# Optimization experiments

Measured on AMD Instinct MI355X. Metric: run time of the kernel, lower is better.

Reference implementation:

```python
import jax, jax.numpy as jnp
import numpy as np

NT = 34000      # nodes per type
NTYPES = 3
NMP = 2         # metapaths per node type
E = 300000      # metapath instances per metapath
L = 3           # metapath length
H = 8           # attention heads
D = 64          # hidden_dim (per-head dim)
HD = H * D      # 512
AV = 128        # attn_vec_dim
C = 8           # out_dim (classes)
NTGT = 1000
NLAYERS = 2
N = NTYPES * NT


def _glorot(k, shape, fan_in):
    return jax.random.normal(k, shape, jnp.float32) * (1.0 / np.sqrt(fan_in))


def setup_inputs() -> dict:
    key = jax.random.key(0)
    ks = jax.random.split(key, 24)
    X0 = jax.random.normal(ks[0], (NT, 512), jnp.float32)
    X1 = jax.random.normal(ks[1], (NT, 256), jnp.float32)
    X2 = jax.random.normal(ks[2], (NT, 128), jnp.float32)
    # metapath instances: column 0 is the target node (must be of type i),
    # remaining columns are intermediate nodes of any type
    dst = jax.random.randint(ks[3], (NTYPES, NMP, E), 0, NT) + jnp.arange(NTYPES)[:, None, None] * NT
    mids = jax.random.randint(ks[4], (NTYPES, NMP, E, L - 1), 0, N)
    mp_idx = jnp.concatenate([dst[..., None], mids], axis=-1).astype(jnp.int32)
    target_idx = jax.random.randint(ks[5], (NTGT,), 0, NT).astype(jnp.int32)
    inp = {
        "X0": X0, "X1": X1, "X2": X2,
        # per-type feature transforms (fc_list)
        "fcW0": _glorot(ks[6], (512, D), 512), "fcb0": jnp.zeros((D,), jnp.float32),
        "fcW1": _glorot(ks[7], (256, D), 256), "fcb1": jnp.zeros((D,), jnp.float32),
        "fcW2": _glorot(ks[8], (128, D), 128), "fcb2": jnp.zeros((D,), jnp.float32),
        # GAT-style intra-metapath attention params [layer, type, metapath, H, D]
        "attn1": jax.random.normal(ks[9], (NLAYERS, NTYPES, NMP, H, D), jnp.float32) * 0.1,
        "attn2": jax.random.normal(ks[10], (NLAYERS, NTYPES, NMP, H, D), jnp.float32) * 0.1,
        # inter-metapath attention (fc1 + attention vector q) [layer, type, ...]
        "mpW": _glorot(ks[11], (NLAYERS, NTYPES, HD, AV), HD),
        "mpb": jnp.zeros((NLAYERS, NTYPES, AV), jnp.float32),
        "mpq": jax.random.normal(ks[12], (NLAYERS, NTYPES, AV), jnp.float32) * 0.1,
        # per-layer output fc: in_dim*num_heads -> out_dim
        "lW0": _glorot(ks[13], (HD, D), HD), "lb0": jnp.zeros((D,), jnp.float32),
        "lW1": _glorot(ks[14], (HD, C), HD), "lb1": jnp.zeros((C,), jnp.float32),
        "mp_idx": mp_idx,
        "target_idx": target_idx,
    }
    return inp


def _ctr_layer(h, a1, a2, mpW, mpb, mpq, mp_idx):
    # one MAGNN_nc_layer ctr-ntype pass: gather metapath instances, intra-metapath
    # attention (segment softmax over target node), inter-metapath attention,
    # then scatter per-type results into the shared node tensor (contiguous blocks).
    outs = []
    for i in range(NTYPES):
        per_mp = []
        for p in range(NMP):
            idx = mp_idx[i, p]                      # [E, L]
            feats = h[idx]                          # [E, L, D] irregular gather
            hid = feats.mean(axis=1)                # rnn_type='average' metapath encoding
            dst = idx[:, 0] - i * NT                # local target-node ids
            e = jax.nn.leaky_relu(
                jnp.einsum('ed,hd->eh', feats[:, 0, :], a1[i, p])
                + jnp.einsum('ed,hd->eh', hid, a2[i, p]), 0.2)   # [E, H]
            m = jax.ops.segment_max(e, dst, num_segments=NT)
            ex = jnp.exp(e - m[dst])
            den = jax.ops.segment_sum(ex, dst, num_segments=NT)
            alpha = ex / jnp.maximum(den[dst], 1e-9)             # segment softmax
            out = jax.ops.segment_sum(alpha[:, :, None] * hid[:, None, :], dst,
                                      num_segments=NT)           # [NT, H, D]
            per_mp.append(jax.nn.elu(out.reshape(NT, HD)))
        st = jnp.stack(per_mp)                       # [P, NT, HD]
        s = jnp.tanh(jnp.einsum('pnd,dk->pnk', st, mpW[i]) + mpb[i]).mean(axis=1) @ mpq[i]  # [P]
        beta = jax.nn.softmax(s)
        outs.append(jnp.einsum('p,pnd->nd', beta, st))
    return jnp.concatenate(outs, axis=0)             # scatter back: [N, HD]


def reference(X0, X1, X2, fcW0, fcb0, fcW1, fcb1, fcW2, fcb2,
              attn1, attn2, mpW, mpb, mpq, lW0, lb0, lW1, lb1,
              mp_idx, target_idx):
    # type-masked gather -> per-type linear -> scatter (types are contiguous blocks)
    h = jnp.concatenate([X0 @ fcW0 + fcb0, X1 @ fcW1 + fcb1, X2 @ fcW2 + fcb2], axis=0)
    hm = _ctr_layer(h, attn1[0], attn2[0], mpW[0], mpb[0], mpq[0], mp_idx)
    h = jax.nn.elu(hm @ lW0 + lb0)                   # layer 0: HD -> hidden, ELU
    hm = _ctr_layer(h, attn1[1], attn2[1], mpW[1], mpb[1], mpq[1], mp_idx)
    logits = hm @ lW1 + lb1                          # final layer: HD -> out_dim
    return logits[target_idx]
```

## Files before the change

kernel.cpp:

```cpp
#include <hip/hip_runtime.h>
#include <hip/hip_bf16.h>
#include <math.h>

#define NT 34000
#define NTYPES 3
#define NMP 2
#define NE 300000
#define HH 8
#define DD 64
#define HD 512
#define AV 128
#define NCLS 8
#define NTGT 1000
#define NN (NTYPES*NT)
#define NBLK 133

typedef short short8 __attribute__((ext_vector_type(8)));
typedef float f32x4 __attribute__((ext_vector_type(4)));

__device__ __forceinline__ short f2bf(float f){
  unsigned u = __float_as_uint(f);
  unsigned r = u + 0x7FFFu + ((u>>16)&1u);
  return (short)(r>>16);
}
__device__ __forceinline__ float bf2f(short s){
  return __uint_as_float(((unsigned)(unsigned short)s)<<16);
}
__device__ __forceinline__ float fast_tanh(float x){
  x = fminf(15.f, fmaxf(-15.f, x));
  float t = __expf(2.f*x);
  return (t-1.f)/(t+1.f);
}

__device__ __forceinline__ void compute_beta(const float* __restrict__ av,
                                             const float* __restrict__ q,
                                             float* b0, float* b1){
  float s0=0.f, s1=0.f;
  #pragma unroll
  for(int c=0;c<32;c++){
    float4 a0=((const float4*)av)[c];
    float4 a1=((const float4*)(av+128))[c];
    float4 qq=((const float4*)q)[c];
    s0 += a0.x*qq.x+a0.y*qq.y+a0.z*qq.z+a0.w*qq.w;
    s1 += a1.x*qq.x+a1.y*qq.y+a1.z*qq.z+a1.w*qq.w;
  }
  s0 /= (float)NT; s1 /= (float)NT;
  float mm=fmaxf(s0,s1);
  float e0=__expf(s0-mm), e1=__expf(s1-mm);
  float d=e0+e1;
  *b0=e0/d; *b1=e1/d;
}

__global__ void k_zero(int* __restrict__ p, int n){
  int i = blockIdx.x*256+threadIdx.x; if(i<n) p[i]=0;
}

__global__ void k_hist(const int* __restrict__ mp, int* __restrict__ counts){
  int e = blockIdx.x*256+threadIdx.x; int g = blockIdx.y;
  if(e>=NE) return;
  int i = g>>1;
  int dst = mp[((size_t)g*NE+e)*3] - i*NT;
  atomicAdd(&counts[g*NT+dst],1);
}

__global__ __launch_bounds__(256) void k_blkred(const int* __restrict__ counts, int* __restrict__ bsum){
  int g=blockIdx.y, blk=blockIdx.x, t=threadIdx.x;
  int idx=blk*256+t;
  int v=(idx<NT)? counts[g*NT+idx]:0;
  #pragma unroll
  for(int off=32;off;off>>=1) v+=__shfl_down(v,off,64);
  __shared__ int sh[4];
  if((t&63)==0) sh[t>>6]=v;
  __syncthreads();
  if(t==0) bsum[g*NBLK+blk]=sh[0]+sh[1]+sh[2]+sh[3];
}

__global__ __launch_bounds__(256) void k_scansums(int* __restrict__ bsum){
  int g=blockIdx.x; int t=threadIdx.x;
  __shared__ int s[256];
  int v=(t<NBLK)? bsum[g*NBLK+t]:0;
  s[t]=v; __syncthreads();
  for(int off=1;off<256;off<<=1){
    int tmp=(t>=off)?s[t-off]:0; __syncthreads();
    s[t]+=tmp; __syncthreads();
  }
  if(t<NBLK) bsum[g*NBLK+t]=s[t]-v;
}

__global__ __launch_bounds__(256) void k_scanapply(int* __restrict__ counts, const int* __restrict__ bsum,
                                                   int* __restrict__ offs){
  int g=blockIdx.y, blk=blockIdx.x, t=threadIdx.x;
  int idx=blk*256+t;
  int v=(idx<NT)? counts[g*NT+idx]:0;
  __shared__ int s[256];
  s[t]=v; __syncthreads();
  for(int off=1;off<256;off<<=1){
    int tmp=(t>=off)?s[t-off]:0; __syncthreads();
    s[t]+=tmp; __syncthreads();
  }
  int excl = s[t]-v + bsum[g*NBLK+blk];
  if(idx<NT){ offs[g*(NT+1)+idx]=excl; counts[g*NT+idx]=0; }
  if(idx==NT-1) offs[g*(NT+1)+NT]=excl+v;
}

__global__ void k_scatter(const int* __restrict__ mp, const int* __restrict__ offs,
                          int* __restrict__ counts, int2* __restrict__ mids){
  int e = blockIdx.x*256+threadIdx.x; int g=blockIdx.y;
  if(e>=NE) return;
  int i=g>>1;
  const int* row = mp + ((size_t)g*NE+e)*3;
  int dst = row[0]-i*NT;
  int pos = offs[g*(NT+1)+dst] + atomicAdd(&counts[g*NT+dst],1);
  mids[(size_t)g*NE+pos]=make_int2(row[1],row[2]);
}

__global__ void k_packWall(const float* __restrict__ W0, const float* __restrict__ W1,
                           const float* __restrict__ W2, const float* __restrict__ WL,
                           const float* __restrict__ mpW,
                           short* __restrict__ p0, short* __restrict__ p1,
                           short* __restrict__ p2, short* __restrict__ pL,
                           short* __restrict__ bpk4, float* __restrict__ accv){
  int which = blockIdx.y;
  int tid = blockIdx.x*256+threadIdx.x;
  if(which<4){
    const float* W; short* wpk; int K;
    if(which==0){W=W0;wpk=p0;K=512;}
    else if(which==1){W=W1;wpk=p1;K=256;}
    else if(which==2){W=W2;wpk=p2;K=128;}
    else {W=WL;wpk=pL;K=512;}
    int nk = K>>5;
    int total = nk*256;
    if(tid>=total) return;
    int lane = tid&63; int c=(tid>>6)&3; int kt=tid>>8;
    int col = c*16 + (lane&15);
    int kbase = kt*32 + ((lane>>4)<<3);
    short8 hi, lo;
    #pragma unroll
    for(int j=0;j<8;j++){
      float w = W[(size_t)(kbase+j)*64+col];
      short h = f2bf(w); hi[j]=h;
      lo[j] = f2bf(w - bf2f(h));
    }
    ((short8*)wpk)[tid] = hi;
    ((short8*)wpk)[total+tid] = lo;
  } else {
    if(which==4 && tid<1024) accv[tid]=0.f;
    if(tid>=8192) return;
    const float* W = mpW + (size_t)(which-4)*512*128;
    short* out = bpk4 + (size_t)(which-4)*65536;
    int lane=tid&63; int c=(tid>>6)&7; int t=tid>>9;
    int kbase = t*32 + ((lane>>4)<<3);
    int col = c*16 + (lane&15);
    short8 v;
    #pragma unroll
    for(int jj=0;jj<8;jj++) v[jj]=f2bf(W[(size_t)(kbase+jj)*128+col]);
    ((short8*)out)[tid]=v;
  }
}

__global__ __launch_bounds__(256) void k_mm64f(const float* __restrict__ X, const short* __restrict__ wpk,
               const float* __restrict__ b, float* __restrict__ Y, short* __restrict__ Yb,
               int rows, int K, int act){
  int wave = threadIdx.x>>6, lane = threadIdx.x&63;
  int row0 = blockIdx.x*64 + wave*16;
  if(row0>=rows) return;
  int r = row0 + (lane&15);
  int rc = min(r, rows-1);
  const float* xr = X + (size_t)rc*K + ((lane>>4)<<3);
  int nk = K>>5;
  const short8* wh = (const short8*)wpk;
  const short8* wl = wh + (size_t)nk*256;
  f32x4 acc[4];
  #pragma unroll
  for(int c=0;c<4;c++) acc[c]=(f32x4){0.f,0.f,0.f,0.f};
  for(int kt=0;kt<nk;kt++){
    float4 f0=*(const float4*)(xr + kt*32);
    float4 f1=*(const float4*)(xr + kt*32 + 4);
    float xs[8]={f0.x,f0.y,f0.z,f0.w,f1.x,f1.y,f1.z,f1.w};
    short8 ah, al;
    #pragma unroll
    for(int j=0;j<8;j++){
      short h=f2bf(xs[j]); ah[j]=h;
      al[j]=f2bf(xs[j]-bf2f(h));
    }
    const short8* whk = wh + (size_t)kt*256 + lane;
    const short8* wlk = wl + (size_t)kt*256 + lane;
    #pragma unroll
    for(int c=0;c<4;c++){
      short8 bh = whk[c*64];
      short8 bl = wlk[c*64];
      acc[c]=__builtin_amdgcn_mfma_f32_16x16x32_bf16(ah,bh,acc[c],0,0,0);
      acc[c]=__builtin_amdgcn_mfma_f32_16x16x32_bf16(al,bh,acc[c],0,0,0);
      acc[c]=__builtin_amdgcn_mfma_f32_16x16x32_bf16(ah,bl,acc[c],0,0,0);
    }
  }
  int rbase = row0 + ((lane>>4)<<2);
  int colb = lane&15;
  #pragma unroll
  for(int c=0;c<4;c++){
    int col = c*16+colb;
    float bb = b[col];
    #pragma unroll
    for(int q=0;q<4;q++){
      int rw = rbase+q;
      if(rw<rows){
        float v = acc[c][q]+bb;
        if(act) v = v>0.f? v : (__expf(v)-1.f);
        Y[(size_t)rw*64+col]=v;
        Yb[(size_t)rw*64+col]=f2bf(v);
      }
    }
  }
}

__global__ __launch_bounds__(256) void k_mm64fB(const short* __restrict__ Xa, const short* __restrict__ Xb,
               const float* __restrict__ accv_s, const float* __restrict__ q,
               const short* __restrict__ wpk,
               const float* __restrict__ b, float* __restrict__ Y, int rows, int act){
  const int K=512, nk=16;
  float b0, b1;
  compute_beta(accv_s, q, &b0, &b1);
  int wave = threadIdx.x>>6, lane = threadIdx.x&63;
  int row0 = blockIdx.x*64 + wave*16;
  if(row0>=rows) return;
  int r = row0 + (lane&15);
  int rc = min(r, rows-1);
  const short* xra = Xa + (size_t)rc*K + ((lane>>4)<<3);
  const short* xrb = Xb + (size_t)rc*K + ((lane>>4)<<3);
  const short8* wh = (const short8*)wpk;
  const short8* wl = wh + (size_t)nk*256;
  f32x4 acc[4];
  #pragma unroll
  for(int c=0;c<4;c++) acc[c]=(f32x4){0.f,0.f,0.f,0.f};
  for(int kt=0;kt<nk;kt++){
    short8 sa = *(const short8*)(xra + kt*32);
    short8 sb = *(const short8*)(xrb + kt*32);
    short8 ah, al;
    #pragma unroll
    for(int j=0;j<8;j++){
      float x = b0*bf2f(sa[j]) + b1*bf2f(sb[j]);
      short h=f2bf(x); ah[j]=h;
      al[j]=f2bf(x-bf2f(h));
    }
    const short8* whk = wh + (size_t)kt*256 + lane;
    const short8* wlk = wl + (size_t)kt*256 + lane;
    #pragma unroll
    for(int c=0;c<4;c++){
      short8 bh = whk[c*64];
      short8 bl = wlk[c*64];
      acc[c]=__builtin_amdgcn_mfma_f32_16x16x32_bf16(ah,bh,acc[c],0,0,0);
      acc[c]=__builtin_amdgcn_mfma_f32_16x16x32_bf16(al,bh,acc[c],0,0,0);
      acc[c]=__builtin_amdgcn_mfma_f32_16x16x32_bf16(ah,bl,acc[c],0,0,0);
    }
  }
  int rbase = row0 + ((lane>>4)<<2);
  int colb = lane&15;
  #pragma unroll
  for(int c=0;c<4;c++){
    int col = c*16+colb;
    float bb = b[col];
    #pragma unroll
    for(int q=0;q<4;q++){
      int rw = rbase+q;
      if(rw<rows){
        float v = acc[c][q]+bb;
        if(act) v = v>0.f? v : (__expf(v)-1.f);
        Y[(size_t)rw*64+col]=v;
      }
    }
  }
}

__global__ __launch_bounds__(256) void k_cvt(const float* __restrict__ src, short* __restrict__ dst, int n8){
  int i = blockIdx.x*256+threadIdx.x;
  if(i>=n8) return;
  float4 f0=((const float4*)src)[i*2], f1=((const float4*)src)[i*2+1];
  short8 v;
  v[0]=f2bf(f0.x); v[1]=f2bf(f0.y); v[2]=f2bf(f0.z); v[3]=f2bf(f0.w);
  v[4]=f2bf(f1.x); v[5]=f2bf(f1.y); v[6]=f2bf(f1.z); v[7]=f2bf(f1.w);
  ((short8*)dst)[i]=v;
}

__global__ __launch_bounds__(256) void k_pre(const float* __restrict__ h, const float* __restrict__ a1,
              const float* __restrict__ a2, float* __restrict__ ptab, int ngroups){
  int node = blockIdx.x*256+threadIdx.x;
  if(node>=NN) return;
  const float* hr = h + (size_t)node*64;
  float4 hv[16];
  #pragma unroll
  for(int q=0;q<16;q++) hv[q]=((const float4*)hr)[q];
  for(int g=0; g<ngroups; g++){
    const float* A1 = a1 + (size_t)g*512;
    const float* A2 = a2 + (size_t)g*512;
    float out[16];
    #pragma unroll
    for(int o=0;o<8;o++){
      float acc=0.f;
      #pragma unroll
      for(int q=0;q<16;q++){
        float4 w=((const float4*)A1)[o*16+q];
        acc += hv[q].x*w.x+hv[q].y*w.y+hv[q].z*w.z+hv[q].w*w.w;
      }
      out[o]=acc;
    }
    #pragma unroll
    for(int o=0;o<8;o++){
      float acc=0.f;
      #pragma unroll
      for(int q=0;q<16;q++){
        float4 w=((const float4*)A2)[o*16+q];
        acc += hv[q].x*w.x+hv[q].y*w.y+hv[q].z*w.z+hv[q].w*w.w;
      }
      out[8+o]=acc;
    }
    float* dp = ptab + ((size_t)g*NN+node)*16;
    #pragma unroll
    for(int q=0;q<4;q++)
      ((float4*)dp)[q]=make_float4(out[q*4],out[q*4+1],out[q*4+2],out[q*4+3]);
  }
}

__global__ __launch_bounds__(256) void k_seg(const int* __restrict__ offs_all, const float* __restrict__ ptab,
   const int2* __restrict__ mids_all, const float* __restrict__ h, const short* __restrict__ hb,
   short* __restrict__ stb, float* __restrict__ stf, int type, int tobf){
  __shared__ float wsh[4][64];
  int wave = threadIdx.x>>6, lane = threadIdx.x&63;
  int n = blockIdx.x*4 + wave;
  if(n>=NT) return;
  int p = blockIdx.y; int g = type*2+p;
  const int* offs = offs_all + (size_t)g*(NT+1);
  const int2* mids_g = mids_all + (size_t)g*NE;
  const float* pt = ptab + (size_t)g*NN*16;
  const unsigned short* hbp = (const unsigned short*)hb;

  int off = offs[n], end = offs[n+1];
  const float third = 1.f/3.f;
  int j = lane>>3, hh = lane&7;

  const float* pn = pt + (size_t)(type*NT+n)*16;
  float baseh = pn[hh] + pn[8+hh]*third;

  float m = -1e30f, den = 0.f;
  for(int s=off+j; s<end; s+=8){
    int2 mm = mids_g[s];
    float q1 = pt[(size_t)mm.x*16 + 8 + hh];
    float q2 = pt[(size_t)mm.y*16 + 8 + hh];
    float e = baseh + (q1+q2)*third;
    float ev = e>0.f? e : 0.2f*e;
    float mn = fmaxf(m, ev);
    den = den*__expf(m-mn) + __expf(ev-mn);
    m = mn;
  }
  #pragma unroll
  for(int o8=8;o8<=32;o8<<=1){
    float om = __shfl_xor(m, o8, 64);
    float od = __shfl_xor(den, o8, 64);
    float mn = fmaxf(m, om);
    den = den*__expf(m-mn) + od*__expf(om-mn);
    m = mn;
  }
  float invD = 1.f/fmaxf(den, 1e-9f);

  float o[8]={0.f,0.f,0.f,0.f,0.f,0.f,0.f,0.f};
  for(int base=off; base<end; base+=8){
    int s = base+j;
    float w = 0.f;
    if(s<end){
      int2 mm = mids_g[s];
      float q1 = pt[(size_t)mm.x*16 + 8 + hh];
      float q2 = pt[(size_t)mm.y*16 + 8 + hh];
      float e = baseh + (q1+q2)*third;
      float ev = e>0.f? e : 0.2f*e;
      w = __expf(ev-m)*invD;
    }
    wsh[wave][lane] = w;
    int cnt = min(8, end-base);
    for(int k=0;k<cnt;k++){
      int2 mm = mids_g[base+k];
      unsigned ux = hbp[(size_t)mm.x*64+lane];
      unsigned uy = hbp[(size_t)mm.y*64+lane];
      float hvm = __uint_as_float(ux<<16) + __uint_as_float(uy<<16);
      float4 a0 = *(const float4*)&wsh[wave][k*8];
      float4 a1 = *(const float4*)&wsh[wave][k*8+4];
      o[0]+=a0.x*hvm; o[1]+=a0.y*hvm; o[2]+=a0.z*hvm; o[3]+=a0.w*hvm;
      o[4]+=a1.x*hvm; o[5]+=a1.y*hvm; o[6]+=a1.z*hvm; o[7]+=a1.w*hvm;
    }
  }

  float hn = h[((size_t)type*NT+(size_t)n)*64+lane];
  short* stbp = stb + (size_t)p*NT*512 + (size_t)n*512 + lane;
  float* stfp = stf + (size_t)p*NT*512 + (size_t)n*512 + lane;
  #pragma unroll
  for(int q=0;q<8;q++){
    float v = (end>off)? (o[q] + hn)*third : 0.f;
    v = v>0.f? v : (__expf(v)-1.f);
    if(tobf) stbp[q*64] = f2bf(v);
    else     stfp[q*64] = v;
  }
}

__global__ __launch_bounds__(256) void k_tanhmm(const short* __restrict__ stb, const float* __restrict__ stf,
                        int isbf, const short* __restrict__ bpk,
                        const float* __restrict__ bias, float* __restrict__ accv_s){
  __shared__ float red[4][128];
  int wave=threadIdx.x>>6, lane=threadIdx.x&63;
  int p=blockIdx.y;
  int row0 = (blockIdx.x*4+wave)*16;
  int active = (row0<NT);
  int rA = row0 + (lane&15); if(rA>NT-1) rA=NT-1;
  const short* arowb = stb + (size_t)p*NT*512 + (size_t)rA*512 + ((lane>>4)<<3);
  const float* arowf = stf + (size_t)p*NT*512 + (size_t)rA*512 + ((lane>>4)<<3);
  f32x4 acc[8];
  #pragma unroll
  for(int c=0;c<8;c++) acc[c]=(f32x4){0.f,0.f,0.f,0.f};
  const short8* bp = (const short8*)bpk;
  if(active){
    for(int kt=0;kt<16;kt++){
      short8 a;
      if(isbf){
        a = *(const short8*)(arowb + kt*32);
      } else {
        float4 f0 = *(const float4*)(arowf + kt*32);
        float4 f1 = *(const float4*)(arowf + kt*32 + 4);
        a[0]=f2bf(f0.x); a[1]=f2bf(f0.y); a[2]=f2bf(f0.z); a[3]=f2bf(f0.w);
        a[4]=f2bf(f1.x); a[5]=f2bf(f1.y); a[6]=f2bf(f1.z); a[7]=f2bf(f1.w);
      }
      const short8* bk = bp + (size_t)kt*512 + lane;
      #pragma unroll
      for(int c=0;c<8;c++){
        short8 bfr = bk[c*64];
        acc[c]=__builtin_amdgcn_mfma_f32_16x16x32_bf16(a,bfr,acc[c],0,0,0);
      }
    }
  }
  int rbase = row0 + ((lane>>4)<<2);
  int colb = lane&15;
  float sc[8];
  #pragma unroll
  for(int c=0;c<8;c++){
    float s=0.f;
    if(active){
      float bb=bias[c*16+colb];
      #pragma unroll
      for(int r=0;r<4;r++){
        if(rbase+r<NT) s += fast_tanh(acc[c][r]+bb);
      }
    }
    s += __shfl_xor(s,16,64);
    s += __shfl_xor(s,32,64);
    sc[c]=s;
  }
  if(lane<16){
    #pragma unroll
    for(int c=0;c<8;c++) red[wave][c*16+lane]=sc[c];
  }
  __syncthreads();
  if(threadIdx.x<128){
    float t = red[0][threadIdx.x]+red[1][threadIdx.x]+red[2][threadIdx.x]+red[3][threadIdx.x];
    atomicAdd(&accv_s[p*128+threadIdx.x], t);
  }
}

__global__ __launch_bounds__(64) void k_final(const float* __restrict__ st0, const float* __restrict__ st1,
      const float* __restrict__ accv_s, const float* __restrict__ q,
      const float* __restrict__ lW1, const float* __restrict__ lb1,
      const int* __restrict__ tgt, float* __restrict__ out){
  int t=blockIdx.x; int lane=threadIdx.x;
  int row=tgt[t];
  float b0, b1;
  compute_beta(accv_s, q, &b0, &b1);
  float acc[8]={0.f,0.f,0.f,0.f,0.f,0.f,0.f,0.f};
  #pragma unroll
  for(int kk=0;kk<8;kk++){
    int k=kk*64+lane;
    float hm=b0*st0[(size_t)row*512+k]+b1*st1[(size_t)row*512+k];
    const float4* wp=(const float4*)(lW1+(size_t)k*8);
    float4 w0=wp[0], w1=wp[1];
    acc[0]+=hm*w0.x; acc[1]+=hm*w0.y; acc[2]+=hm*w0.z; acc[3]+=hm*w0.w;
    acc[4]+=hm*w1.x; acc[5]+=hm*w1.y; acc[6]+=hm*w1.z; acc[7]+=hm*w1.w;
  }
  #pragma unroll
  for(int c=0;c<8;c++){
    #pragma unroll
    for(int off=32;off>0;off>>=1) acc[c]+=__shfl_xor(acc[c],off,64);
  }
  if(lane<8){
    float v=0.f;
    #pragma unroll
    for(int c=0;c<8;c++) if(lane==c) v=acc[c];
    out[t*8+lane]=v+lb1[lane];
  }
}

extern "C" void kernel_launch(void* const* d_in, const int* in_sizes, int n_in,
                              void* d_out, int out_size, void* d_ws, size_t ws_size,
                              hipStream_t stream) {
  const float* X0=(const float*)d_in[0];
  const float* X1=(const float*)d_in[1];
  const float* X2=(const float*)d_in[2];
  const float* fcW0=(const float*)d_in[3]; const float* fcb0=(const float*)d_in[4];
  const float* fcW1=(const float*)d_in[5]; const float* fcb1=(const float*)d_in[6];
  const float* fcW2=(const float*)d_in[7]; const float* fcb2=(const float*)d_in[8];
  const float* attn1=(const float*)d_in[9];
  const float* attn2=(const float*)d_in[10];
  const float* mpW=(const float*)d_in[11];
  const float* mpb=(const float*)d_in[12];
  const float* mpq=(const float*)d_in[13];
  const float* lW0=(const float*)d_in[14]; const float* lb0=(const float*)d_in[15];
  const float* lW1=(const float*)d_in[16]; const float* lb1=(const float*)d_in[17];
  const int* mp=(const int*)d_in[18];
  const int* tgt=(const int*)d_in[19];
  float* out=(float*)d_out;

  char* ws=(char*)d_ws;
  float* h0   =(float*)(ws+0);
  float* h1   =(float*)(ws+26112000);
  float* ptab =(float*)(ws+52224000);
  int*   offs =(int*  )(ws+91392000);
  int*   counts=(int* )(ws+92208128);
  int2*  mids =(int2* )(ws+100224128);
  short* hb   =(short*)(ws+114624128);
  short* stb  =(short*)(ws+133824128);
  float* stf  =(float*)(ws+133824128);
  short* bpk4 =(short*)(ws+273088128);
  float* accv =(float*)(ws+273612416);
  short* wpk0 =(short*)(ws+92208128);
  short* wpk1 =(short*)(ws+92339200);
  short* wpkL =(short*)(ws+92404736);
  short* wpk2 =(short*)(ws+92535808);
  int*   bsum =(int*  )(ws+133824128);

  dim3 b256(256);
  k_zero<<<dim3((6*NT+255)/256),b256,0,stream>>>(counts,6*NT);
  k_hist<<<dim3((NE+255)/256,6),b256,0,stream>>>(mp,counts);
  k_blkred<<<dim3(NBLK,6),b256,0,stream>>>(counts,bsum);
  k_scansums<<<dim3(6),b256,0,stream>>>(bsum);
  k_scanapply<<<dim3(NBLK,6),b256,0,stream>>>(counts,bsum,offs);
  k_scatter<<<dim3((NE+255)/256,6),b256,0,stream>>>(mp,offs,counts,mids);

  k_packWall<<<dim3(32,8),b256,0,stream>>>(fcW0,fcW1,fcW2,lW0,mpW,wpk0,wpk1,wpk2,wpkL,bpk4,accv);

  k_mm64f<<<dim3(532),b256,0,stream>>>(X0,wpk0,fcb0,h0,hb,NT,512,0);
  k_mm64f<<<dim3(532),b256,0,stream>>>(X1,wpk1,fcb1,h0+(size_t)NT*64,hb+(size_t)NT*64,NT,256,0);
  k_mm64f<<<dim3(532),b256,0,stream>>>(X2,wpk2,fcb2,h0+(size_t)2*NT*64,hb+(size_t)2*NT*64,NT,128,0);

  k_pre<<<dim3((NN+255)/256),b256,0,stream>>>(h0,attn1,attn2,ptab,6);
  for(int type=0;type<3;type++){
    k_seg<<<dim3(NT/4,2),b256,0,stream>>>(offs,ptab,mids,h0,hb,stb,stf,type,1);
    k_tanhmm<<<dim3(532,2),b256,0,stream>>>(stb,stf,1,bpk4+(size_t)type*65536,
                                            mpb+(0*3+type)*128,accv+type*256);
    k_mm64fB<<<dim3(532),b256,0,stream>>>(stb,stb+(size_t)NT*512,accv+type*256,mpq+(0*3+type)*128,
                                          wpkL,lb0,h1+(size_t)type*NT*64,NT,1);
  }

  k_cvt<<<dim3((NN*64/8+255)/256),b256,0,stream>>>(h1,hb,NN*64/8);
  k_pre<<<dim3((NN+255)/256),b256,0,stream>>>(h1,attn1+(size_t)6*512,attn2+(size_t)6*512,ptab,2);
  k_seg<<<dim3(NT/4,2),b256,0,stream>>>(offs,ptab,mids,h1,hb,stb,stf,0,0);
  k_tanhmm<<<dim3(532,2),b256,0,stream>>>(stb,stf,0,bpk4+(size_t)3*65536,
                                          mpb+(1*3+0)*128,accv+3*256);
  k_final<<<dim3(NTGT),dim3(64),0,stream>>>(stf,stf+(size_t)NT*512,accv+3*256,mpq+(1*3+0)*128,
                                            lW1,lb1,tgt,out);
}
```

Before: 1.178 ms.

## Co-schedule CSR scatter with feature matmuls and fold bf16 conversion into k_pre

```diff
diff --git a/kernel.cpp b/kernel.cpp
--- a/kernel.cpp
+++ b/kernel.cpp
@@ -14,6 +14,9 @@
 #define NTGT 1000
 #define NN (NTYPES*NT)
 #define NBLK 133
+#define SCBLK 1172
+#define TSC (6*SCBLK)
+#define TMM (3*532)
 
 typedef short short8 __attribute__((ext_vector_type(8)));
 typedef float f32x4 __attribute__((ext_vector_type(4)));
@@ -101,17 +104,6 @@
   int excl = s[t]-v + bsum[g*NBLK+blk];
   if(idx<NT){ offs[g*(NT+1)+idx]=excl; counts[g*NT+idx]=0; }
   if(idx==NT-1) offs[g*(NT+1)+NT]=excl+v;
-}
-
-__global__ void k_scatter(const int* __restrict__ mp, const int* __restrict__ offs,
-                          int* __restrict__ counts, int2* __restrict__ mids){
-  int e = blockIdx.x*256+threadIdx.x; int g=blockIdx.y;
-  if(e>=NE) return;
-  int i=g>>1;
-  const int* row = mp + ((size_t)g*NE+e)*3;
-  int dst = row[0]-i*NT;
-  int pos = offs[g*(NT+1)+dst] + atomicAdd(&counts[g*NT+dst],1);
-  mids[(size_t)g*NE+pos]=make_int2(row[1],row[2]);
 }
 
 __global__ void k_packWall(const float* __restrict__ W0, const float* __restrict__ W1,
@@ -158,14 +150,38 @@
   }
 }
 
-__global__ __launch_bounds__(256) void k_mm64f(const float* __restrict__ X, const short* __restrict__ wpk,
-               const float* __restrict__ b, float* __restrict__ Y, short* __restrict__ Yb,
-               int rows, int K, int act){
+__global__ __launch_bounds__(256) void k_scmm(const int* __restrict__ mp, const int* __restrict__ offs,
+    int* __restrict__ counts, int2* __restrict__ mids,
+    const float* __restrict__ X0, const float* __restrict__ X1, const float* __restrict__ X2,
+    const short* __restrict__ wpk0, const short* __restrict__ wpk1, const short* __restrict__ wpk2,
+    const float* __restrict__ fb0, const float* __restrict__ fb1, const float* __restrict__ fb2,
+    float* __restrict__ Y, short* __restrict__ Yb){
+  int bid = blockIdx.x;
+  int period = bid/27, r = bid - period*27;
+  if(r<22){
+    int s = period*22 + r; if(s>=TSC) return;
+    int g = s/SCBLK; int e = (s - g*SCBLK)*256 + threadIdx.x;
+    if(e>=NE) return;
+    int i = g>>1;
+    const int* row = mp + ((size_t)g*NE+e)*3;
+    int dst = row[0]-i*NT;
+    int pos = offs[g*(NT+1)+dst] + atomicAdd(&counts[g*NT+dst],1);
+    mids[(size_t)g*NE+pos]=make_int2(row[1],row[2]);
+    return;
+  }
+  int mID = period*5 + (r-22); if(mID>=TMM) return;
+  int which = mID/532; int xb = mID - which*532;
+  const float* X; const short* wpk; const float* b; int K;
+  if(which==0){X=X0;wpk=wpk0;b=fb0;K=512;}
+  else if(which==1){X=X1;wpk=wpk1;b=fb1;K=256;}
+  else {X=X2;wpk=wpk2;b=fb2;K=128;}
+  float* Yw = Y + (size_t)which*NT*64;
+  short* Ybw = Yb + (size_t)which*NT*64;
   int wave = threadIdx.x>>6, lane = threadIdx.x&63;
-  int row0 = blockIdx.x*64 + wave*16;
-  if(row0>=rows) return;
-  int r = row0 + (lane&15);
-  int rc = min(r, rows-1);
+  int row0 = xb*64 + wave*16;
+  if(row0>=NT) return;
+  int rr = row0 + (lane&15);
+  int rc = min(rr, NT-1);
   const float* xr = X + (size_t)rc*K + ((lane>>4)<<3);
   int nk = K>>5;
   const short8* wh = (const short8*)wpk;
@@ -203,11 +219,10 @@
     #pragma unroll
     for(int q=0;q<4;q++){
       int rw = rbase+q;
-      if(rw<rows){
+      if(rw<NT){
         float v = acc[c][q]+bb;
-        if(act) v = v>0.f? v : (__expf(v)-1.f);
-        Y[(size_t)rw*64+col]=v;
-        Yb[(size_t)rw*64+col]=f2bf(v);
+        Yw[(size_t)rw*64+col]=v;
+        Ybw[(size_t)rw*64+col]=f2bf(v);
       }
     }
   }
@@ -271,24 +286,26 @@
   }
 }
 
-__global__ __launch_bounds__(256) void k_cvt(const float* __restrict__ src, short* __restrict__ dst, int n8){
-  int i = blockIdx.x*256+threadIdx.x;
-  if(i>=n8) return;
-  float4 f0=((const float4*)src)[i*2], f1=((const float4*)src)[i*2+1];
-  short8 v;
-  v[0]=f2bf(f0.x); v[1]=f2bf(f0.y); v[2]=f2bf(f0.z); v[3]=f2bf(f0.w);
-  v[4]=f2bf(f1.x); v[5]=f2bf(f1.y); v[6]=f2bf(f1.z); v[7]=f2bf(f1.w);
-  ((short8*)dst)[i]=v;
-}
-
 __global__ __launch_bounds__(256) void k_pre(const float* __restrict__ h, const float* __restrict__ a1,
-              const float* __restrict__ a2, float* __restrict__ ptab, int ngroups){
+              const float* __restrict__ a2, float* __restrict__ ptab, int ngroups,
+              short* __restrict__ hbout){
   int node = blockIdx.x*256+threadIdx.x;
   if(node>=NN) return;
   const float* hr = h + (size_t)node*64;
   float4 hv[16];
   #pragma unroll
   for(int q=0;q<16;q++) hv[q]=((const float4*)hr)[q];
+  if(hbout){
+    short* hp = hbout + (size_t)node*64;
+    #pragma unroll
+    for(int qq=0;qq<8;qq++){
+      float4 a=hv[2*qq], b4=hv[2*qq+1];
+      short8 v;
+      v[0]=f2bf(a.x); v[1]=f2bf(a.y); v[2]=f2bf(a.z); v[3]=f2bf(a.w);
+      v[4]=f2bf(b4.x); v[5]=f2bf(b4.y); v[6]=f2bf(b4.z); v[7]=f2bf(b4.w);
+      ((short8*)hp)[qq]=v;
+    }
+  }
   for(int g=0; g<ngroups; g++){
     const float* A1 = a1 + (size_t)g*512;
     const float* A2 = a2 + (size_t)g*512;
@@ -520,14 +537,14 @@
   int*   counts=(int* )(ws+92208128);
   int2*  mids =(int2* )(ws+100224128);
   short* hb   =(short*)(ws+114624128);
+  short* wpk0 =(short*)(ws+127680128);
+  short* wpk1 =(short*)(ws+127811200);
+  short* wpkL =(short*)(ws+127876736);
+  short* wpk2 =(short*)(ws+128007808);
   short* stb  =(short*)(ws+133824128);
   float* stf  =(float*)(ws+133824128);
   short* bpk4 =(short*)(ws+273088128);
   float* accv =(float*)(ws+273612416);
-  short* wpk0 =(short*)(ws+92208128);
-  short* wpk1 =(short*)(ws+92339200);
-  short* wpkL =(short*)(ws+92404736);
-  short* wpk2 =(short*)(ws+92535808);
   int*   bsum =(int*  )(ws+133824128);
 
   dim3 b256(256);
@@ -536,15 +553,13 @@
   k_blkred<<<dim3(NBLK,6),b256,0,stream>>>(counts,bsum);
   k_scansums<<<dim3(6),b256,0,stream>>>(bsum);
   k_scanapply<<<dim3(NBLK,6),b256,0,stream>>>(counts,bsum,offs);
-  k_scatter<<<dim3((NE+255)/256,6),b256,0,stream>>>(mp,offs,counts,mids);
 
   k_packWall<<<dim3(32,8),b256,0,stream>>>(fcW0,fcW1,fcW2,lW0,mpW,wpk0,wpk1,wpk2,wpkL,bpk4,accv);
 
-  k_mm64f<<<dim3(532),b256,0,stream>>>(X0,wpk0,fcb0,h0,hb,NT,512,0);
-  k_mm64f<<<dim3(532),b256,0,stream>>>(X1,wpk1,fcb1,h0+(size_t)NT*64,hb+(size_t)NT*64,NT,256,0);
-  k_mm64f<<<dim3(532),b256,0,stream>>>(X2,wpk2,fcb2,h0+(size_t)2*NT*64,hb+(size_t)2*NT*64,NT,128,0);
-
-  k_pre<<<dim3((NN+255)/256),b256,0,stream>>>(h0,attn1,attn2,ptab,6);
+  k_scmm<<<dim3(320*27),b256,0,stream>>>(mp,offs,counts,mids,X0,X1,X2,
+                                         wpk0,wpk1,wpk2,fcb0,fcb1,fcb2,h0,hb);
+
+  k_pre<<<dim3((NN+255)/256),b256,0,stream>>>(h0,attn1,attn2,ptab,6,(short*)nullptr);
   for(int type=0;type<3;type++){
     k_seg<<<dim3(NT/4,2),b256,0,stream>>>(offs,ptab,mids,h0,hb,stb,stf,type,1);
     k_tanhmm<<<dim3(532,2),b256,0,stream>>>(stb,stf,1,bpk4+(size_t)type*65536,
@@ -553,8 +568,7 @@
                                           wpkL,lb0,h1+(size_t)type*NT*64,NT,1);
   }
 
-  k_cvt<<<dim3((NN*64/8+255)/256),b256,0,stream>>>(h1,hb,NN*64/8);
-  k_pre<<<dim3((NN+255)/256),b256,0,stream>>>(h1,attn1+(size_t)6*512,attn2+(size_t)6*512,ptab,2);
+  k_pre<<<dim3((NN+255)/256),b256,0,stream>>>(h1,attn1+(size_t)6*512,attn2+(size_t)6*512,ptab,2,hb);
   k_seg<<<dim3(NT/4,2),b256,0,stream>>>(offs,ptab,mids,h1,hb,stb,stf,0,0);
   k_tanhmm<<<dim3(532,2),b256,0,stream>>>(stb,stf,0,bpk4+(size_t)3*65536,
                                           mpb+(1*3+0)*128,accv+3*256);
```

New measurement: 1.126 ms. 1.05x faster.
